# Kernel tuning notes

Measured on AMD Instinct MI355X. Metric: run time of the kernel, lower is better.

Reference implementation:

```python
import jax, jax.numpy as jnp
import numpy as np

DIM_QK = 256
SCALE = DIM_QK ** (-0.5)


def _nearest_resize(mask, H, W):
    # torch F.interpolate(mode='nearest'): src_idx = floor(dst_idx * in/out)
    B, C, h, w = mask.shape
    ri = (jnp.arange(H) * h) // H
    ci = (jnp.arange(W) * w) // W
    return mask[:, :, ri[:, None], ci[None, :]]  # [B,C,H,W]


def setup_inputs() -> dict:
    key = jax.random.key(0)
    ks = jax.random.split(key, 9)
    B, C, H, W = 2, 256, 64, 64
    return {
        "queries": jax.random.normal(ks[0], (B, C, H, W), jnp.float32),
        "keys": jax.random.normal(ks[1], (B, C, H, W), jnp.float32),
        "values": jax.random.normal(ks[2], (B, C, H, W), jnp.float32),
        "mask_eye": jax.random.uniform(ks[3], (B, 1, 128, 128), jnp.float32),
        "mask_mouth": jax.random.uniform(ks[4], (B, 1, 128, 128), jnp.float32),
        "q_pos": jax.random.normal(ks[5], (1, H * W, C), jnp.float32),
        "k_pos": jax.random.normal(ks[6], (1, H * W, C), jnp.float32),
        "bias_eye": jax.random.normal(ks[7], (1,), jnp.float32),
        "bias_mouth": jax.random.normal(ks[8], (1,), jnp.float32),
    }


def reference(queries, keys, values, mask_eye, mask_mouth, q_pos, k_pos, bias_eye, bias_mouth):
    B, C, H, W = queries.shape
    N = H * W
    q = queries.reshape(B, C, N).transpose(0, 2, 1) + q_pos  # [B,N,C]
    k = keys.reshape(B, C, N).transpose(0, 2, 1) + k_pos
    v = values.reshape(B, C, N).transpose(0, 2, 1)
    dots = jnp.einsum('bnc,bmc->bnm', q, k) * SCALE  # [B,N,N]
    attn = jax.nn.softmax(dots, axis=-1)
    # post-softmax mask-derived additive bias (order: eye then mouth,
    # matching self.bias=[bias_eye, bias_mouth] vs mask_list order)
    for mask, b in ((mask_eye, bias_eye), (mask_mouth, bias_mouth)):
        m = _nearest_resize(mask, H, W).reshape(B, 1, N)  # [B,1,N]
        # torch.matmul(m, m^T) with m [B,1,N] -> [B,1,1] (per-batch inner product)
        mask_map = jnp.sum(m * m, axis=-1, keepdims=True)[..., None][:, :, 0]  # [B,1,1]
        attn = attn + jax.nn.softplus(b * mask_map)
    out = jnp.einsum('bnm,bmc->bnc', attn, v)  # [B,N,C]
    return out.transpose(0, 2, 1).reshape(values.shape)
```

## Files before the change

### kernel.cpp

```cpp
#include <hip/hip_runtime.h>

typedef float f32x4 __attribute__((ext_vector_type(4)));
typedef int   i32x4 __attribute__((ext_vector_type(4)));
typedef short bf16x8 __attribute__((ext_vector_type(8)));

#define MFMA16(a, b, c) __builtin_amdgcn_mfma_f32_16x16x32_bf16((a), (b), (c), 0, 0, 0)

#define NN 4096
#define DD 256
#define SCALE 0.0625f
#define THR 8.0f

static __device__ __forceinline__ unsigned short f2bf(float f) {
  unsigned int u = __float_as_uint(f);
  u += 0x7FFFu + ((u >> 16) & 1u);
  return (unsigned short)(u >> 16);
}

static __device__ __forceinline__ unsigned pack2bf(float lo, float hi) {
  return (unsigned)f2bf(lo) | ((unsigned)f2bf(hi) << 16);
}

static __device__ __forceinline__ float bf2f(unsigned short u) {
  return __uint_as_float((unsigned)u << 16);
}

static __device__ __forceinline__ float softplusf(float x) {
  return (x > 20.f) ? x : log1pf(__expf(x));
}

__global__ __launch_bounds__(256) void prep_qk(
    const float* __restrict__ q, const float* __restrict__ k,
    const float* __restrict__ qp, const float* __restrict__ kp,
    unsigned short* __restrict__ qbf, unsigned short* __restrict__ kbf) {
  int n0 = blockIdx.x * 32, c0 = blockIdx.y * 32;
  int b = blockIdx.z & 1, which = blockIdx.z >> 1;
  const float* src = which ? k : q;
  const float* pos = which ? kp : qp;
  unsigned short* dst = which ? kbf : qbf;
  float scl = which ? 1.0f : SCALE;

  __shared__ float tile[32][33];
  int tx = threadIdx.x & 31, ty = threadIdx.x >> 5;
#pragma unroll
  for (int i = 0; i < 4; ++i) {
    int c = c0 + ty + i * 8;
    tile[ty + i * 8][tx] = src[((size_t)(b * DD + c)) * NN + n0 + tx];
  }
  __syncthreads();
#pragma unroll
  for (int i = 0; i < 4; ++i) {
    int n = n0 + ty + i * 8;
    float v = (tile[tx][ty + i * 8] + pos[(size_t)n * DD + c0 + tx]) * scl;
    dst[((size_t)(b * NN + n)) * DD + c0 + tx] = f2bf(v);
  }
}

__global__ __launch_bounds__(256) void prep_v(
    const float* __restrict__ src, unsigned short* __restrict__ vbf,
    float* __restrict__ colsum) {
  int row = blockIdx.x;
  const float* s = src + (size_t)row * NN;
  unsigned short* d = vbf + (size_t)row * NN;
  int tid = threadIdx.x;
  float sum = 0.f;
#pragma unroll
  for (int i = 0; i < 16; ++i) {
    int n = tid + i * 256;
    float v = s[n];
    sum += v;
    d[n] = f2bf(v);
  }
#pragma unroll
  for (int off = 1; off < 64; off <<= 1) sum += __shfl_xor(sum, off);
  __shared__ float ps[4];
  if ((tid & 63) == 0) ps[tid >> 6] = sum;
  __syncthreads();
  if (tid == 0) colsum[row] = ps[0] + ps[1] + ps[2] + ps[3];
}

__global__ __launch_bounds__(256) void prep_mask(
    const float* __restrict__ me, const float* __restrict__ mm,
    float* __restrict__ msums) {
  int b = blockIdx.x >> 1, which = blockIdx.x & 1;
  const float* m = which ? mm : me;
  int tid = threadIdx.x;
  float sum = 0.f;
#pragma unroll
  for (int i = 0; i < 16; ++i) {
    int p = tid + i * 256;
    int y = p >> 6, x = p & 63;
    float v = m[(size_t)(b * 128 + 2 * y) * 128 + 2 * x];
    sum += v * v;
  }
#pragma unroll
  for (int off = 1; off < 64; off <<= 1) sum += __shfl_xor(sum, off);
  __shared__ float ps[4];
  if ((tid & 63) == 0) ps[tid >> 6] = sum;
  __syncthreads();
  if (tid == 0) msums[blockIdx.x] = ps[0] + ps[1] + ps[2] + ps[3];
}

static __device__ __forceinline__ void load_k(
    const unsigned short* __restrict__ kb, int kvb, int wid, int lane, i32x4* kr) {
  int krow = wid * 8 + (lane >> 3);
  int kc = lane & 7;
  const unsigned short* kp = kb + (size_t)(kvb + krow) * DD;
#pragma unroll
  for (int i = 0; i < 4; ++i)
    kr[i] = *(const i32x4*)(kp + ((kc | (i << 3)) << 3));
}

static __device__ __forceinline__ void load_v(
    const unsigned short* __restrict__ vb, int kvb, int wid, int lane, i32x4* vr) {
  int vd = wid * 64 + lane;
  const unsigned short* vp = vb + (size_t)vd * NN + kvb;
#pragma unroll
  for (int i = 0; i < 4; ++i)
    vr[i] = *(const i32x4*)(vp + (i << 3));
}

static __device__ __forceinline__ void write_k(
    char* kdst, int wid, int lane, const i32x4* kr) {
  int krow = wid * 8 + (lane >> 3);
  int kc = lane & 7;
  int prow = ((krow & 4) << 2) | ((krow >> 3) << 2) | (krow & 3);
  int rx = prow & 7;
#pragma unroll
  for (int i = 0; i < 4; ++i)
    *(i32x4*)(kdst + prow * 512 + (((kc | (i << 3)) ^ rx) << 4)) = kr[i];
}

static __device__ __forceinline__ void write_v(
    char* vdst, int wid, int lane, const i32x4* vr) {
  int vd = wid * 64 + lane;
  int vx = (vd >> 1) & 3;
#pragma unroll
  for (int i = 0; i < 4; ++i)
    *(i32x4*)(vdst + vd * 64 + ((i ^ vx) << 4)) = vr[i];
}

static __device__ __forceinline__ void compute_qk(
    const unsigned short* __restrict__ Kc, const bf16x8* qB, int ll, int lg,
    f32x4* st) {
  st[0] = (f32x4){0.f, 0.f, 0.f, 0.f};
  st[1] = (f32x4){0.f, 0.f, 0.f, 0.f};
  __builtin_amdgcn_s_setprio(1);
#pragma unroll
  for (int t = 0; t < 2; ++t) {
    int row = t * 16 + ll;
    int rx = row & 7;
    const unsigned short* krd = Kc + row * 256;
#pragma unroll
    for (int kd = 0; kd < 8; ++kd) {
      bf16x8 kf = *(const bf16x8*)(krd + ((((kd << 2) | lg) ^ rx) << 3));
      st[t] = MFMA16(kf, qB[kd], st[t]);
    }
  }
  __builtin_amdgcn_s_setprio(0);
}

__global__ __launch_bounds__(256, 2) void attn_partial(
    const unsigned short* __restrict__ qbf,
    const unsigned short* __restrict__ kbf,
    const unsigned short* __restrict__ vbf,
    unsigned short* __restrict__ opartb, float* __restrict__ mlpart, int ks) {
  int hwb = blockIdx.x;
  int bid = (hwb & 7) * ((int)gridDim.x >> 3) + (hwb >> 3);
  int qblk = bid & 63;
  int combo = bid >> 6;
  int b = combo / ks, sidx = combo % ks;
  int kvlen = NN / ks;
  int kv0 = sidx * kvlen;
  int nt = kvlen >> 5;

  int tid = threadIdx.x, wid = tid >> 6, lane = tid & 63;
  int ll = lane & 15, lg = lane >> 4;
  int qt16 = qblk * 4 + wid;

  __shared__ __align__(16) unsigned short Klds[2][32 * 256];
  __shared__ __align__(16) unsigned short Vlds[3][256 * 32];

  const unsigned short* kb = kbf + (size_t)b * NN * DD;
  const unsigned short* vb = vbf + (size_t)b * DD * NN;

  bf16x8 qB[8];
  {
    const unsigned short* qp0 = qbf + ((size_t)b * NN + (size_t)qt16 * 16) * DD;
#pragma unroll
    for (int kd = 0; kd < 8; ++kd)
      qB[kd] = *(const bf16x8*)(qp0 + (size_t)ll * DD + kd * 32 + lg * 8);
  }

  f32x4 o[16];
#pragma unroll
  for (int db = 0; db < 16; ++db) o[db] = (f32x4){0.f, 0.f, 0.f, 0.f};
  float m_ref = -1e30f;
  float sum_lane = 0.f;

  i32x4 kr[4], vr[4];
  load_k(kb, kv0, wid, lane, kr);
  load_v(vb, kv0, wid, lane, vr);
  write_k((char*)&Klds[0][0], wid, lane, kr);
  write_v((char*)&Vlds[0][0], wid, lane, vr);
  if (nt > 1) {
    load_k(kb, kv0 + 32, wid, lane, kr);
    load_v(vb, kv0 + 32, wid, lane, vr);
    write_k((char*)&Klds[1][0], wid, lane, kr);
    write_v((char*)&Vlds[1][0], wid, lane, vr);
  }
  __syncthreads();

  f32x4 st[2];
  compute_qk(&Klds[0][0], qB, ll, lg, st);
  __syncthreads();

  int vp = 0;
  int wp = 2;

  for (int tt = 0; tt < nt; ++tt) {
    bool have1 = (tt + 1 < nt);
    bool have2 = (tt + 2 < nt);
    if (have2) {
      load_k(kb, kv0 + (tt + 2) * 32, wid, lane, kr);
      load_v(vb, kv0 + (tt + 2) * 32, wid, lane, vr);
    }

    float tm = fmaxf(fmaxf(fmaxf(st[0][0], st[0][1]), fmaxf(st[0][2], st[0][3])),
                     fmaxf(fmaxf(st[1][0], st[1][1]), fmaxf(st[1][2], st[1][3])));
    if (__any(tm > m_ref + THR)) {
      float tq = fmaxf(tm, __shfl_xor(tm, 16));
      tq = fmaxf(tq, __shfl_xor(tq, 32));
      float mn = fmaxf(m_ref, tq);
      float sc = __expf(m_ref - mn);
      sum_lane *= sc;
      m_ref = mn;
#pragma unroll
      for (int r = 0; r < 4; ++r) {
        float sv = __shfl(sc, (lg << 2) + r);
#pragma unroll
        for (int db = 0; db < 16; ++db) o[db][r] *= sv;
      }
    }

    f32x4 stn[2];
    if (have1) compute_qk(&Klds[(tt + 1) & 1][0], qB, ll, lg, stn);

    unsigned pk[2][2];
#pragma unroll
    for (int t = 0; t < 2; ++t) {
      float a0 = __expf(st[t][0] - m_ref);
      float a1 = __expf(st[t][1] - m_ref);
      float a2 = __expf(st[t][2] - m_ref);
      float a3 = __expf(st[t][3] - m_ref);
      sum_lane += (a0 + a1) + (a2 + a3);
      pk[t][0] = pack2bf(a0, a1);
      pk[t][1] = pack2bf(a2, a3);
    }
    i32x4 fi = (i32x4){(int)pk[0][0], (int)pk[0][1], (int)pk[1][0], (int)pk[1][1]};
    bf16x8 pa = __builtin_bit_cast(bf16x8, fi);

    const unsigned short* Vc = &Vlds[vp][0];
    __builtin_amdgcn_s_setprio(1);
#pragma unroll
    for (int db = 0; db < 16; ++db) {
      int d = (db << 4) + ll;
      bf16x8 vf = *(const bf16x8*)(Vc + d * 32 + ((lg ^ ((d >> 1) & 3)) << 3));
      o[db] = MFMA16(pa, vf, o[db]);
    }
    __builtin_amdgcn_s_setprio(0);

    if (have2) {
      write_k((char*)&Klds[tt & 1][0], wid, lane, kr);
      write_v((char*)&Vlds[wp][0], wid, lane, vr);
    }
    __syncthreads();

    if (have1) { st[0] = stn[0]; st[1] = stn[1]; }
    vp = (vp == 2) ? 0 : vp + 1;
    wp = (wp == 2) ? 0 : wp + 1;
  }

  sum_lane += __shfl_xor(sum_lane, 16);
  sum_lane += __shfl_xor(sum_lane, 32);

  size_t slot = (size_t)(b * 256 + qt16) * ks + sidx;
  unsigned short* op = opartb + slot * 4096;
#pragma unroll
  for (int db = 0; db < 16; ++db) {
    unsigned u0 = pack2bf(o[db][0], o[db][1]);
    unsigned u1 = pack2bf(o[db][2], o[db][3]);
    unsigned* p = (unsigned*)&op[(size_t)((db * 16 + ll) * 16 + lg * 4)];
    p[0] = u0;
    p[1] = u1;
  }
  if (lg == 0) {
    float* mlp = mlpart + slot * 32;
    mlp[ll * 2 + 0] = m_ref;
    mlp[ll * 2 + 1] = sum_lane;
  }
}

__global__ __launch_bounds__(256) void attn_combine(
    const unsigned short* __restrict__ opartb, const float* __restrict__ mlpart,
    const float* __restrict__ colsum, const float* __restrict__ msums,
    const float* __restrict__ bias_eye, const float* __restrict__ bias_mouth,
    float* __restrict__ out, int ks) {
  int gb = blockIdx.x;
  int b = gb >> 8, qt16 = gb & 255;
  int tid = threadIdx.x;
  __shared__ float wtab[8][16];
  size_t slot0 = (size_t)(b * 256 + qt16) * ks;

  if (tid < 16) {
    int q = tid;
    float m[8], l[8], w[8];
    float M = -1e30f;
#pragma unroll
    for (int s = 0; s < 8; ++s) {
      if (s < ks) {
        m[s] = mlpart[(slot0 + s) * 32 + q * 2 + 0];
        l[s] = mlpart[(slot0 + s) * 32 + q * 2 + 1];
        M = fmaxf(M, m[s]);
      } else { m[s] = -1e30f; l[s] = 0.f; }
    }
    float L = 0.f;
#pragma unroll
    for (int s = 0; s < 8; ++s) {
      w[s] = (s < ks) ? __expf(m[s] - M) : 0.f;
      L += l[s] * w[s];
    }
    float invL = 1.f / L;
#pragma unroll
    for (int s = 0; s < 8; ++s) wtab[s][q] = w[s] * invL;
  }
  __syncthreads();

  int d = tid;
  float sb = softplusf(bias_eye[0] * msums[b * 2 + 0]) +
             softplusf(bias_mouth[0] * msums[b * 2 + 1]);
  float cs = colsum[b * DD + d] * sb;

  float acc[16];
#pragma unroll
  for (int q = 0; q < 16; ++q) acc[q] = cs;

#pragma unroll
  for (int s = 0; s < 8; ++s) {
    if (s < ks) {
      const unsigned short* op = opartb + (slot0 + s) * 4096 + d * 16;
#pragma unroll
      for (int q = 0; q < 16; ++q)
        acc[q] += wtab[s][q] * bf2f(op[q]);
    }
  }

  float* ob = out + ((size_t)(b * DD + d)) * NN + qt16 * 16;
#pragma unroll
  for (int g = 0; g < 4; ++g) {
    f32x4 v = (f32x4){acc[g * 4 + 0], acc[g * 4 + 1], acc[g * 4 + 2], acc[g * 4 + 3]};
    *(f32x4*)&ob[g * 4] = v;
  }
}

extern "C" void kernel_launch(void* const* d_in, const int* in_sizes, int n_in,
                              void* d_out, int out_size, void* d_ws, size_t ws_size,
                              hipStream_t stream) {
  (void)in_sizes; (void)n_in; (void)out_size;
  const float* queries    = (const float*)d_in[0];
  const float* keys       = (const float*)d_in[1];
  const float* values     = (const float*)d_in[2];
  const float* mask_eye   = (const float*)d_in[3];
  const float* mask_mouth = (const float*)d_in[4];
  const float* q_pos      = (const float*)d_in[5];
  const float* k_pos      = (const float*)d_in[6];
  const float* bias_eye   = (const float*)d_in[7];
  const float* bias_mouth = (const float*)d_in[8];
  float* out = (float*)d_out;

  char* w = (char*)d_ws;
  unsigned short* qbf = (unsigned short*)(w);
  unsigned short* kbf = (unsigned short*)(w + ((size_t)4 << 20));
  unsigned short* vbf = (unsigned short*)(w + ((size_t)8 << 20));
  float* colsum = (float*)(w + ((size_t)12 << 20));
  float* msums  = (float*)(w + ((size_t)12 << 20) + 4096);

  const size_t opart_off = ((size_t)12 << 20) + 8192;
  const size_t opart_chunk = (size_t)512 * 8192;
  const size_t ml_chunk = (size_t)512 * 128;

  int ks = 1;
  for (int cand = 8; cand >= 1; cand >>= 1) {
    if (ws_size >= opart_off + (size_t)cand * (opart_chunk + ml_chunk)) { ks = cand; break; }
  }

  unsigned short* opartp = (unsigned short*)(w + opart_off);
  float* mlp = (float*)(w + opart_off + (size_t)ks * opart_chunk);

  prep_qk<<<dim3(128, 8, 4), 256, 0, stream>>>(queries, keys, q_pos, k_pos, qbf, kbf);
  prep_v<<<512, 256, 0, stream>>>(values, vbf, colsum);
  prep_mask<<<4, 256, 0, stream>>>(mask_eye, mask_mouth, msums);

  attn_partial<<<128 * ks, 256, 0, stream>>>(qbf, kbf, vbf, opartp, mlp, ks);
  attn_combine<<<512, 256, 0, stream>>>(opartp, mlp, colsum, msums,
                                        bias_eye, bias_mouth, out, ks);
}
```

Before: 86.94 us.

## Process two query tiles per wave to reuse K/V fragments, simplify pipeline

Each wave now handles 32 query rows, two 16-row tiles, instead of 16. Every K and V fragment read from LDS then feeds two MFMAs, which halves LDS traffic and global K/V loads per query and halves the grid. The three-stage software pipeline, which computed QK for the next tile ahead and used a triple V buffer, is replaced by a simpler double-buffered loop with launch bounds of 1 block per CU. The cost is doubled accumulator registers, lower occupancy, fewer blocks to fill the CUs, and less overlap between loads and compute.

```diff
diff --git a/kernel.cpp b/kernel.cpp
--- a/kernel.cpp
+++ b/kernel.cpp
@@ -140,35 +140,15 @@
     *(i32x4*)(vdst + vd * 64 + ((i ^ vx) << 4)) = vr[i];
 }
 
-static __device__ __forceinline__ void compute_qk(
-    const unsigned short* __restrict__ Kc, const bf16x8* qB, int ll, int lg,
-    f32x4* st) {
-  st[0] = (f32x4){0.f, 0.f, 0.f, 0.f};
-  st[1] = (f32x4){0.f, 0.f, 0.f, 0.f};
-  __builtin_amdgcn_s_setprio(1);
-#pragma unroll
-  for (int t = 0; t < 2; ++t) {
-    int row = t * 16 + ll;
-    int rx = row & 7;
-    const unsigned short* krd = Kc + row * 256;
-#pragma unroll
-    for (int kd = 0; kd < 8; ++kd) {
-      bf16x8 kf = *(const bf16x8*)(krd + ((((kd << 2) | lg) ^ rx) << 3));
-      st[t] = MFMA16(kf, qB[kd], st[t]);
-    }
-  }
-  __builtin_amdgcn_s_setprio(0);
-}
-
-__global__ __launch_bounds__(256, 2) void attn_partial(
+__global__ __launch_bounds__(256, 1) void attn_partial(
     const unsigned short* __restrict__ qbf,
     const unsigned short* __restrict__ kbf,
     const unsigned short* __restrict__ vbf,
     unsigned short* __restrict__ opartb, float* __restrict__ mlpart, int ks) {
   int hwb = blockIdx.x;
   int bid = (hwb & 7) * ((int)gridDim.x >> 3) + (hwb >> 3);
-  int qblk = bid & 63;
-  int combo = bid >> 6;
+  int qblk = bid & 31;
+  int combo = bid >> 5;
   int b = combo / ks, sidx = combo % ks;
   int kvlen = NN / ks;
   int kv0 = sidx * kvlen;
@@ -176,128 +156,151 @@
 
   int tid = threadIdx.x, wid = tid >> 6, lane = tid & 63;
   int ll = lane & 15, lg = lane >> 4;
-  int qt16 = qblk * 4 + wid;
+  int qt32 = qblk * 4 + wid;
 
   __shared__ __align__(16) unsigned short Klds[2][32 * 256];
-  __shared__ __align__(16) unsigned short Vlds[3][256 * 32];
+  __shared__ __align__(16) unsigned short Vlds[2][256 * 32];
 
   const unsigned short* kb = kbf + (size_t)b * NN * DD;
   const unsigned short* vb = vbf + (size_t)b * DD * NN;
 
-  bf16x8 qB[8];
+  bf16x8 qB[2][8];
   {
-    const unsigned short* qp0 = qbf + ((size_t)b * NN + (size_t)qt16 * 16) * DD;
-#pragma unroll
-    for (int kd = 0; kd < 8; ++kd)
-      qB[kd] = *(const bf16x8*)(qp0 + (size_t)ll * DD + kd * 32 + lg * 8);
-  }
-
-  f32x4 o[16];
-#pragma unroll
-  for (int db = 0; db < 16; ++db) o[db] = (f32x4){0.f, 0.f, 0.f, 0.f};
-  float m_ref = -1e30f;
-  float sum_lane = 0.f;
+    const unsigned short* qp0 = qbf + ((size_t)b * NN + (size_t)qt32 * 32) * DD;
+#pragma unroll
+    for (int h = 0; h < 2; ++h)
+#pragma unroll
+      for (int kd = 0; kd < 8; ++kd)
+        qB[h][kd] = *(const bf16x8*)(qp0 + (size_t)(h * 16 + ll) * DD + kd * 32 + lg * 8);
+  }
+
+  f32x4 o[2][16];
+#pragma unroll
+  for (int h = 0; h < 2; ++h)
+#pragma unroll
+    for (int db = 0; db < 16; ++db) o[h][db] = (f32x4){0.f, 0.f, 0.f, 0.f};
+  float m_ref[2] = {-1e30f, -1e30f};
+  float sum_lane[2] = {0.f, 0.f};
 
   i32x4 kr[4], vr[4];
   load_k(kb, kv0, wid, lane, kr);
   load_v(vb, kv0, wid, lane, vr);
   write_k((char*)&Klds[0][0], wid, lane, kr);
   write_v((char*)&Vlds[0][0], wid, lane, vr);
-  if (nt > 1) {
-    load_k(kb, kv0 + 32, wid, lane, kr);
-    load_v(vb, kv0 + 32, wid, lane, vr);
-    write_k((char*)&Klds[1][0], wid, lane, kr);
-    write_v((char*)&Vlds[1][0], wid, lane, vr);
-  }
   __syncthreads();
 
-  f32x4 st[2];
-  compute_qk(&Klds[0][0], qB, ll, lg, st);
-  __syncthreads();
-
-  int vp = 0;
-  int wp = 2;
-
+  int buf = 0;
   for (int tt = 0; tt < nt; ++tt) {
-    bool have1 = (tt + 1 < nt);
-    bool have2 = (tt + 2 < nt);
-    if (have2) {
-      load_k(kb, kv0 + (tt + 2) * 32, wid, lane, kr);
-      load_v(vb, kv0 + (tt + 2) * 32, wid, lane, vr);
-    }
-
-    float tm = fmaxf(fmaxf(fmaxf(st[0][0], st[0][1]), fmaxf(st[0][2], st[0][3])),
-                     fmaxf(fmaxf(st[1][0], st[1][1]), fmaxf(st[1][2], st[1][3])));
-    if (__any(tm > m_ref + THR)) {
-      float tq = fmaxf(tm, __shfl_xor(tm, 16));
-      tq = fmaxf(tq, __shfl_xor(tq, 32));
-      float mn = fmaxf(m_ref, tq);
-      float sc = __expf(m_ref - mn);
-      sum_lane *= sc;
-      m_ref = mn;
+    bool more = (tt + 1 < nt);
+    if (more) load_k(kb, kv0 + (tt + 1) * 32, wid, lane, kr);
+
+    const unsigned short* Kc = &Klds[buf][0];
+
+    f32x4 st[2][2];
+    st[0][0] = (f32x4){0.f, 0.f, 0.f, 0.f};
+    st[0][1] = (f32x4){0.f, 0.f, 0.f, 0.f};
+    st[1][0] = (f32x4){0.f, 0.f, 0.f, 0.f};
+    st[1][1] = (f32x4){0.f, 0.f, 0.f, 0.f};
+    __builtin_amdgcn_s_setprio(1);
+#pragma unroll
+    for (int t = 0; t < 2; ++t) {
+      int row = t * 16 + ll;
+      int rx = row & 7;
+      const unsigned short* krd = Kc + row * 256;
+#pragma unroll
+      for (int kd = 0; kd < 8; ++kd) {
+        bf16x8 kf = *(const bf16x8*)(krd + ((((kd << 2) | lg) ^ rx) << 3));
+        st[0][t] = MFMA16(kf, qB[0][kd], st[0][t]);
+        st[1][t] = MFMA16(kf, qB[1][kd], st[1][t]);
+      }
+    }
+    __builtin_amdgcn_s_setprio(0);
+
+    if (more) {
+      write_k((char*)&Klds[buf ^ 1][0], wid, lane, kr);
+      load_v(vb, kv0 + (tt + 1) * 32, wid, lane, vr);
+    }
+
+    float tm0 = fmaxf(fmaxf(fmaxf(st[0][0][0], st[0][0][1]), fmaxf(st[0][0][2], st[0][0][3])),
+                      fmaxf(fmaxf(st[0][1][0], st[0][1][1]), fmaxf(st[0][1][2], st[0][1][3])));
+    float tm1 = fmaxf(fmaxf(fmaxf(st[1][0][0], st[1][0][1]), fmaxf(st[1][0][2], st[1][0][3])),
+                      fmaxf(fmaxf(st[1][1][0], st[1][1][1]), fmaxf(st[1][1][2], st[1][1][3])));
+    if (__any((tm0 > m_ref[0] + THR) || (tm1 > m_ref[1] + THR))) {
+      float tq0 = fmaxf(tm0, __shfl_xor(tm0, 16));
+      tq0 = fmaxf(tq0, __shfl_xor(tq0, 32));
+      float tq1 = fmaxf(tm1, __shfl_xor(tm1, 16));
+      tq1 = fmaxf(tq1, __shfl_xor(tq1, 32));
+      float mn0 = fmaxf(m_ref[0], tq0), mn1 = fmaxf(m_ref[1], tq1);
+      float sc0 = __expf(m_ref[0] - mn0), sc1 = __expf(m_ref[1] - mn1);
+      sum_lane[0] *= sc0; sum_lane[1] *= sc1;
+      m_ref[0] = mn0; m_ref[1] = mn1;
 #pragma unroll
       for (int r = 0; r < 4; ++r) {
-        float sv = __shfl(sc, (lg << 2) + r);
-#pragma unroll
-        for (int db = 0; db < 16; ++db) o[db][r] *= sv;
+        float sv0 = __shfl(sc0, (lg << 2) + r);
+        float sv1 = __shfl(sc1, (lg << 2) + r);
+#pragma unroll
+        for (int db = 0; db < 16; ++db) { o[0][db][r] *= sv0; o[1][db][r] *= sv1; }
       }
     }
 
-    f32x4 stn[2];
-    if (have1) compute_qk(&Klds[(tt + 1) & 1][0], qB, ll, lg, stn);
-
-    unsigned pk[2][2];
-#pragma unroll
-    for (int t = 0; t < 2; ++t) {
-      float a0 = __expf(st[t][0] - m_ref);
-      float a1 = __expf(st[t][1] - m_ref);
-      float a2 = __expf(st[t][2] - m_ref);
-      float a3 = __expf(st[t][3] - m_ref);
-      sum_lane += (a0 + a1) + (a2 + a3);
-      pk[t][0] = pack2bf(a0, a1);
-      pk[t][1] = pack2bf(a2, a3);
-    }
-    i32x4 fi = (i32x4){(int)pk[0][0], (int)pk[0][1], (int)pk[1][0], (int)pk[1][1]};
-    bf16x8 pa = __builtin_bit_cast(bf16x8, fi);
-
-    const unsigned short* Vc = &Vlds[vp][0];
+    bf16x8 pa[2];
+#pragma unroll
+    for (int h = 0; h < 2; ++h) {
+      unsigned p0, p1, p2, p3;
+      float a0 = __expf(st[h][0][0] - m_ref[h]);
+      float a1 = __expf(st[h][0][1] - m_ref[h]);
+      float a2 = __expf(st[h][0][2] - m_ref[h]);
+      float a3 = __expf(st[h][0][3] - m_ref[h]);
+      float b0 = __expf(st[h][1][0] - m_ref[h]);
+      float b1 = __expf(st[h][1][1] - m_ref[h]);
+      float b2 = __expf(st[h][1][2] - m_ref[h]);
+      float b3 = __expf(st[h][1][3] - m_ref[h]);
+      sum_lane[h] += ((a0 + a1) + (a2 + a3)) + ((b0 + b1) + (b2 + b3));
+      p0 = pack2bf(a0, a1); p1 = pack2bf(a2, a3);
+      p2 = pack2bf(b0, b1); p3 = pack2bf(b2, b3);
+      i32x4 fi = (i32x4){(int)p0, (int)p1, (int)p2, (int)p3};
+      pa[h] = __builtin_bit_cast(bf16x8, fi);
+    }
+
+    const unsigned short* Vc = &Vlds[buf][0];
     __builtin_amdgcn_s_setprio(1);
 #pragma unroll
     for (int db = 0; db < 16; ++db) {
       int d = (db << 4) + ll;
       bf16x8 vf = *(const bf16x8*)(Vc + d * 32 + ((lg ^ ((d >> 1) & 3)) << 3));
-      o[db] = MFMA16(pa, vf, o[db]);
+      o[0][db] = MFMA16(pa[0], vf, o[0][db]);
+      o[1][db] = MFMA16(pa[1], vf, o[1][db]);
     }
     __builtin_amdgcn_s_setprio(0);
 
-    if (have2) {
-      write_k((char*)&Klds[tt & 1][0], wid, lane, kr);
-      write_v((char*)&Vlds[wp][0], wid, lane, vr);
-    }
+    if (more) write_v((char*)&Vlds[buf ^ 1][0], wid, lane, vr);
     __syncthreads();
-
-    if (have1) { st[0] = stn[0]; st[1] = stn[1]; }
-    vp = (vp == 2) ? 0 : vp + 1;
-    wp = (wp == 2) ? 0 : wp + 1;
-  }
-
-  sum_lane += __shfl_xor(sum_lane, 16);
-  sum_lane += __shfl_xor(sum_lane, 32);
-
-  size_t slot = (size_t)(b * 256 + qt16) * ks + sidx;
-  unsigned short* op = opartb + slot * 4096;
-#pragma unroll
-  for (int db = 0; db < 16; ++db) {
-    unsigned u0 = pack2bf(o[db][0], o[db][1]);
-    unsigned u1 = pack2bf(o[db][2], o[db][3]);
-    unsigned* p = (unsigned*)&op[(size_t)((db * 16 + ll) * 16 + lg * 4)];
-    p[0] = u0;
-    p[1] = u1;
-  }
-  if (lg == 0) {
-    float* mlp = mlpart + slot * 32;
-    mlp[ll * 2 + 0] = m_ref;
-    mlp[ll * 2 + 1] = sum_lane;
+    buf ^= 1;
+  }
+
+#pragma unroll
+  for (int h = 0; h < 2; ++h) {
+    sum_lane[h] += __shfl_xor(sum_lane[h], 16);
+    sum_lane[h] += __shfl_xor(sum_lane[h], 32);
+  }
+
+#pragma unroll
+  for (int h = 0; h < 2; ++h) {
+    size_t slot = (size_t)(b * 256 + qt32 * 2 + h) * ks + sidx;
+    unsigned short* op = opartb + slot * 4096;
+#pragma unroll
+    for (int db = 0; db < 16; ++db) {
+      unsigned u0 = pack2bf(o[h][db][0], o[h][db][1]);
+      unsigned u1 = pack2bf(o[h][db][2], o[h][db][3]);
+      unsigned* p = (unsigned*)&op[(size_t)((db * 16 + ll) * 16 + lg * 4)];
+      p[0] = u0;
+      p[1] = u1;
+    }
+    if (lg == 0) {
+      float* mlp = mlpart + slot * 32;
+      mlp[ll * 2 + 0] = m_ref[h];
+      mlp[ll * 2 + 1] = sum_lane[h];
+    }
   }
 }
 
@@ -401,7 +404,7 @@
   prep_v<<<512, 256, 0, stream>>>(values, vbf, colsum);
   prep_mask<<<4, 256, 0, stream>>>(mask_eye, mask_mouth, msums);
 
-  attn_partial<<<128 * ks, 256, 0, stream>>>(qbf, kbf, vbf, opartp, mlp, ks);
+  attn_partial<<<64 * ks, 256, 0, stream>>>(qbf, kbf, vbf, opartp, mlp, ks);
   attn_combine<<<512, 256, 0, stream>>>(opartp, mlp, colsum, msums,
                                         bias_eye, bias_mouth, out, ks);
 }
```

Measured after the change: 105.9 us. 21.9% more time.
